# Performance work log

Measured on AMD Instinct MI355X. Metric: run time of the kernel, lower is better.

The kernel has to match this reference:

```python
import jax, jax.numpy as jnp
import numpy as np

B, L, D, H = 2, 2048, 1024, 16
DH = D // H
NEG = -10000.0

def setup_inputs() -> dict:
    key = jax.random.key(0)
    ks = jax.random.split(key, 6)
    scale = 1.0 / np.sqrt(D)
    inp = {
        "x": jax.random.normal(ks[0], (B, L, D), dtype=jnp.float32),
        "m": jnp.ones((B, L), dtype=jnp.int32),  # 1 = valid token, 0 = padded
        "Wq": jax.random.normal(ks[1], (D, D), dtype=jnp.float32) * scale,
        "bq": jnp.zeros((D,), dtype=jnp.float32),
        "Wk": jax.random.normal(ks[2], (D, D), dtype=jnp.float32) * scale,
        "bk": jnp.zeros((D,), dtype=jnp.float32),
        "Wv": jax.random.normal(ks[3], (D, D), dtype=jnp.float32) * scale,
        "bv": jnp.zeros((D,), dtype=jnp.float32),
        "Wp": jax.random.normal(ks[4], (D, D), dtype=jnp.float32) * scale,
        "bp": jnp.zeros((D,), dtype=jnp.float32),
    }
    return inp

def reference(x, m, Wq, bq, Wk, bk, Wv, bv, Wp, bp):
    # torch Linear: x @ W.T + b
    def heads(t):  # (B,L,D) -> (B,H,L,DH)
        return t.reshape(B, L, H, DH).transpose(0, 2, 1, 3)
    q = heads(x @ Wq.T + bq)
    k = heads(x @ Wk.T + bk)
    v = heads(x @ Wv.T + bv)
    att = jnp.einsum("bhqd,bhkd->bhqk", q, k) * (1.0 / np.sqrt(DH))  # (B,H,L,L)
    causal = jnp.tril(jnp.ones((L, L), dtype=bool))[None, None]       # (1,1,L,L)
    att = jnp.where(causal, att, NEG)
    # additive key-padding mask: 0 for valid, -10000 for padded keys
    pad = (1.0 - m.astype(att.dtype))[:, None, None, :] * NEG         # (B,1,1,L)
    att = att + pad
    att = jax.nn.softmax(att, axis=-1)
    y = jnp.einsum("bhqk,bhkd->bhqd", att, v)                          # (B,H,L,DH)
    y = y.transpose(0, 2, 1, 3).reshape(B, L, D)
    return y @ Wp.T + bp
```

## Files before the change

kernel.cpp:

```cpp
#include <hip/hip_runtime.h>
#include <hip/hip_bf16.h>

#define NB 2
#define NL 2048
#define ND 1024
#define NH 16
#define NDH 64
#define NM (NB*NL)

typedef unsigned short u16;
typedef __attribute__((ext_vector_type(8))) short short8;
typedef __attribute__((ext_vector_type(4))) float floatx4;

__device__ __forceinline__ u16 f2bf(float f) {
  union { float f; unsigned int u; } v; v.f = f;
  unsigned int r = v.u + 0x7FFF + ((v.u >> 16) & 1);
  return (u16)(r >> 16);
}

__device__ __forceinline__ void async_cp16(u16* lds, const u16* g) {
  __builtin_amdgcn_global_load_lds(
      (const __attribute__((address_space(1))) void*)g,
      (__attribute__((address_space(3))) void*)lds, 16, 0, 0);
}

__device__ __forceinline__ unsigned dpp_xor1(unsigned v) {
  return (unsigned)__builtin_amdgcn_mov_dpp((int)v, 0xB1, 0xF, 0xF, true);
}

__global__ __launch_bounds__(256)
void cvt_all(const float* __restrict__ wq, const float* __restrict__ wk,
             const float* __restrict__ wv, const float* __restrict__ wp,
             const float* __restrict__ x,
             u16* __restrict__ ow, u16* __restrict__ ox)
{
  const int per4 = ND * ND / 4;
  const int tot  = 4 * per4 + NM * ND / 4;
  for (int t = blockIdx.x * 256 + threadIdx.x; t < tot; t += gridDim.x * 256) {
    const float* src; uint2* dst; int off;
    if (t < 4 * per4) {
      int w = t >> 18; off = t & (per4 - 1);
      src = (w == 0) ? wq : (w == 1) ? wk : (w == 2) ? wv : wp;
      dst = (uint2*)(ow + (size_t)w * ND * ND);
    } else {
      off = t - 4 * per4; src = x; dst = (uint2*)ox;
    }
    float4 f = ((const float4*)src)[off];
    u16 h[4] = { f2bf(f.x), f2bf(f.y), f2bf(f.z), f2bf(f.w) };
    dst[off] = *(const uint2*)h;
  }
}

#define BM 128
#define BN 128
#define BK 32
#define LDT 32

__global__ __launch_bounds__(256)
void gemm_qkv(const u16* __restrict__ A, const u16* __restrict__ Wb,
              const float* __restrict__ bq, const float* __restrict__ bk,
              const float* __restrict__ bv,
              u16* __restrict__ Qb, u16* __restrict__ Kb, u16* __restrict__ Vb)
{
  const int n0g = blockIdx.x * BN;
  const int z   = n0g >> 10;
  const int n0  = n0g & 1023;
  const u16* W    = Wb + (size_t)z * ND * ND;
  const float* Bi = (z == 0) ? bq : (z == 1) ? bk : bv;
  u16* C          = (z == 0) ? Qb : (z == 1) ? Kb : Vb;
  const float sc  = (z == 0) ? 0.125f : 1.0f;

  const int m0 = blockIdx.y * BM;
  const int tid  = threadIdx.x;
  const int lane = tid & 63;
  const int wave = tid >> 6;
  const int wm = (wave >> 1) * 64;
  const int wn = (wave & 1) * 64;
  const int quad = lane >> 4;
  const int l16  = lane & 15;

  __shared__ u16 As[BM * LDT];
  __shared__ u16 Bs[BN * LDT];

  floatx4 acc[4][4];
#pragma unroll
  for (int i = 0; i < 4; ++i)
#pragma unroll
    for (int j = 0; j < 4; ++j)
      acc[i][j] = (floatx4){0.f, 0.f, 0.f, 0.f};

  for (int k0 = 0; k0 < ND; k0 += BK) {
#pragma unroll
    for (int it = 0; it < 2; ++it) {
      int idx = tid + it * 256;
      int rr  = idx >> 2;
      int c8  = (idx & 3) << 3;
      async_cp16(&Bs[idx * 8], &W[(size_t)(n0 + rr) * ND + k0 + c8]);
      async_cp16(&As[idx * 8], &A[(size_t)(m0 + rr) * ND + k0 + c8]);
    }
    __syncthreads();

    short8 af[4], bfr[4];
#pragma unroll
    for (int i = 0; i < 4; ++i)
      af[i] = *(const short8*)&As[(wm + i * 16 + l16) * LDT + quad * 8];
#pragma unroll
    for (int j = 0; j < 4; ++j)
      bfr[j] = *(const short8*)&Bs[(wn + j * 16 + l16) * LDT + quad * 8];

#pragma unroll
    for (int i = 0; i < 4; ++i)
#pragma unroll
      for (int j = 0; j < 4; ++j)
        acc[i][j] = __builtin_amdgcn_mfma_f32_16x16x32_bf16(af[i], bfr[j], acc[i][j], 0, 0, 0);
    __syncthreads();
  }

#pragma unroll
  for (int j = 0; j < 4; ++j) {
    const int ncol = n0 + wn + j * 16 + l16;
    const float bv2 = Bi[ncol];
#pragma unroll
    for (int i = 0; i < 4; ++i) {
      const int mbase = m0 + wm + i * 16 + quad * 4;
#pragma unroll
      for (int r2 = 0; r2 < 4; ++r2) {
        float v = (acc[i][j][r2] + bv2) * sc;
        C[(size_t)(mbase + r2) * ND + ncol] = f2bf(v);
      }
    }
  }
}

#define BN2 64

__global__ __launch_bounds__(256)
void gemm_proj(const u16* __restrict__ A, const u16* __restrict__ W,
               const float* __restrict__ Bi, float* __restrict__ C)
{
  const int n0 = blockIdx.x * BN2;
  const int m0 = blockIdx.y * BM;
  const int tid  = threadIdx.x;
  const int lane = tid & 63;
  const int wave = tid >> 6;
  const int wm = (wave >> 1) * 64;
  const int wn = (wave & 1) * 32;
  const int quad = lane >> 4;
  const int l16  = lane & 15;

  __shared__ u16 As[BM * LDT];
  __shared__ u16 Bs[BN2 * LDT];

  floatx4 acc[4][2];
#pragma unroll
  for (int i = 0; i < 4; ++i)
#pragma unroll
    for (int j = 0; j < 2; ++j)
      acc[i][j] = (floatx4){0.f, 0.f, 0.f, 0.f};

  for (int k0 = 0; k0 < ND; k0 += BK) {
#pragma unroll
    for (int it = 0; it < 2; ++it) {
      int idx = tid + it * 256;
      int rr  = idx >> 2;
      int c8  = (idx & 3) << 3;
      async_cp16(&As[idx * 8], &A[(size_t)(m0 + rr) * ND + k0 + c8]);
    }
    {
      int rr = tid >> 2, c8 = (tid & 3) << 3;
      async_cp16(&Bs[tid * 8], &W[(size_t)(n0 + rr) * ND + k0 + c8]);
    }
    __syncthreads();

    short8 af[4], bfr[2];
#pragma unroll
    for (int i = 0; i < 4; ++i)
      af[i] = *(const short8*)&As[(wm + i * 16 + l16) * LDT + quad * 8];
#pragma unroll
    for (int j = 0; j < 2; ++j)
      bfr[j] = *(const short8*)&Bs[(wn + j * 16 + l16) * LDT + quad * 8];

#pragma unroll
    for (int i = 0; i < 4; ++i)
#pragma unroll
      for (int j = 0; j < 2; ++j)
        acc[i][j] = __builtin_amdgcn_mfma_f32_16x16x32_bf16(af[i], bfr[j], acc[i][j], 0, 0, 0);
    __syncthreads();
  }

#pragma unroll
  for (int j = 0; j < 2; ++j) {
    const int ncol = n0 + wn + j * 16 + l16;
    const float bv2 = Bi[ncol];
#pragma unroll
    for (int i = 0; i < 4; ++i) {
      const int mbase = m0 + wm + i * 16 + quad * 4;
#pragma unroll
      for (int r2 = 0; r2 < 4; ++r2)
        C[(size_t)(mbase + r2) * ND + ncol] = acc[i][j][r2] + bv2;
    }
  }
}

#define KC 64
#define PSTR 72

__global__ __launch_bounds__(256)
void attn_mfma(const u16* __restrict__ Q, const u16* __restrict__ K,
               const u16* __restrict__ V, const int* __restrict__ msk,
               u16* __restrict__ Y)
{
  const int t = blockIdx.x;
  const int r = t >> 8;
  const int xcd = t & 7;
  const int v = (t >> 3) & 31;
  const int bh = xcd * 4 + r;
  const int qt = (r == 0) ? v
               : (r == 1) ? 31 - v
               : (r == 2) ? ((v + 16) & 31)
                          : ((15 - v) & 31);
  const int b = bh >> 4;
  const int h = bh & 15;
  const int q0 = qt * 64;
  const int tid  = threadIdx.x;
  const int lane = tid & 63;
  const int wave = tid >> 6;
  const int wq   = wave * 16;
  const int quad = lane >> 4;
  const int l16  = lane & 15;

  __shared__ u16 Ks[KC][PSTR];
  __shared__ u16 Vt[NDH][PSTR];
  __shared__ u16 Ps[64][PSTR];
  __shared__ u16 Ms[NL];

  const int nchunks = qt + 1;

  for (int j = tid; j < nchunks * KC; j += 256) Ms[j] = (u16)(msk[b * NL + j] ? 1 : 0);

  short8 qf[2];
#pragma unroll
  for (int kk = 0; kk < 2; ++kk)
    qf[kk] = *(const short8*)&Q[(size_t)(b * NL + q0 + wq + l16) * ND
                                + h * NDH + kk * 32 + quad * 8];

  short8 onesf;
  {
    const short ov = (l16 == 0) ? (short)0x3F80 : (short)0;
#pragma unroll
    for (int e = 0; e < 8; ++e) onesf[e] = ov;
  }

  floatx4 o[4];
#pragma unroll
  for (int ot = 0; ot < 4; ++ot) o[ot] = (floatx4){0.f, 0.f, 0.f, 0.f};
  floatx4 lacc = (floatx4){0.f, 0.f, 0.f, 0.f};

  const int odd = l16 & 1;
  for (int kc = 0; kc < nchunks; ++kc) {
    const int k0 = kc * KC;

#pragma unroll
    for (int p = 0; p < 2; ++p) {
      int idx = tid + p * 256;
      int rr = idx >> 3, c = (idx & 7) << 3;
      *(uint4*)&Ks[rr][c] = *(const uint4*)&K[(size_t)(b * NL + k0 + rr) * ND + h * NDH + c];
    }
    {
      int rv = (tid & 31) * 2;
      int c  = (tid >> 5) * 8;
      uint4 va = *(const uint4*)&V[(size_t)(b * NL + k0 + rv)     * ND + h * NDH + c];
      uint4 vb = *(const uint4*)&V[(size_t)(b * NL + k0 + rv + 1) * ND + h * NDH + c];
      const u16* ap = (const u16*)&va;
      const u16* bp = (const u16*)&vb;
#pragma unroll
      for (int e = 0; e < 8; ++e)
        *(unsigned int*)&Vt[c + e][rv] = (unsigned int)ap[e] | ((unsigned int)bp[e] << 16);
    }
    __syncthreads();

    floatx4 sc[4];
#pragma unroll
    for (int ct = 0; ct < 4; ++ct) {
      short8 kf0 = *(const short8*)&Ks[ct * 16 + l16][quad * 8];
      short8 kf1 = *(const short8*)&Ks[ct * 16 + l16][32 + quad * 8];
      floatx4 a = (floatx4){0.f, 0.f, 0.f, 0.f};
      a = __builtin_amdgcn_mfma_f32_16x16x32_bf16(qf[0], kf0, a, 0, 0, 0);
      a = __builtin_amdgcn_mfma_f32_16x16x32_bf16(qf[1], kf1, a, 0, 0, 0);
      sc[ct] = a;
    }

    const bool diag = (kc == qt);
    const int rowb = q0 + wq + quad * 4;
#pragma unroll
    for (int ct = 0; ct < 4; ++ct) {
      const int col = k0 + ct * 16 + l16;
      const float pmul = (float)Ms[col];
      unsigned bb[4];
#pragma unroll
      for (int r2 = 0; r2 < 4; ++r2) {
        float p = pmul * __expf(sc[ct][r2]);
        if (diag) p = (col > rowb + r2) ? 0.f : p;
        bb[r2] = (unsigned)f2bf(p);
      }
      unsigned n0v = dpp_xor1(bb[0]), n1v = dpp_xor1(bb[1]);
      unsigned n2v = dpp_xor1(bb[2]), n3v = dpp_xor1(bb[3]);
      const int colb  = ct * 16 + (l16 & ~1);
      const int row01 = wq + quad * 4 + odd;
      unsigned d01 = odd ? (n1v | (bb[1] << 16)) : (bb[0] | (n0v << 16));
      unsigned d23 = odd ? (n3v | (bb[3] << 16)) : (bb[2] | (n2v << 16));
      *(unsigned*)&Ps[row01][colb]     = d01;
      *(unsigned*)&Ps[row01 + 2][colb] = d23;
    }

#pragma unroll
    for (int kk = 0; kk < 2; ++kk) {
      short8 pf = *(const short8*)&Ps[wq + l16][kk * 32 + quad * 8];
#pragma unroll
      for (int ot = 0; ot < 4; ++ot) {
        short8 vf = *(const short8*)&Vt[ot * 16 + l16][kk * 32 + quad * 8];
        o[ot] = __builtin_amdgcn_mfma_f32_16x16x32_bf16(pf, vf, o[ot], 0, 0, 0);
      }
      lacc = __builtin_amdgcn_mfma_f32_16x16x32_bf16(pf, onesf, lacc, 0, 0, 0);
    }
    __syncthreads();
  }

  float inv[4];
#pragma unroll
  for (int r2 = 0; r2 < 4; ++r2) {
    const float l = __shfl(lacc[r2], quad << 4);
    inv[r2] = 1.0f / l;
  }
#pragma unroll
  for (int ot = 0; ot < 4; ++ot)
#pragma unroll
    for (int r2 = 0; r2 < 4; ++r2) {
      const int row = q0 + wq + quad * 4 + r2;
      Y[(size_t)(b * NL + row) * ND + h * NDH + ot * 16 + l16] = f2bf(o[ot][r2] * inv[r2]);
    }
}

extern "C" void kernel_launch(void* const* d_in, const int* in_sizes, int n_in,
                              void* d_out, int out_size, void* d_ws, size_t ws_size,
                              hipStream_t stream) {
  const float* x  = (const float*)d_in[0];
  const int*   m  = (const int*)d_in[1];
  const float* Wq = (const float*)d_in[2];
  const float* bq = (const float*)d_in[3];
  const float* Wk = (const float*)d_in[4];
  const float* bk = (const float*)d_in[5];
  const float* Wv = (const float*)d_in[6];
  const float* bv = (const float*)d_in[7];
  const float* Wp = (const float*)d_in[8];
  const float* bp = (const float*)d_in[9];
  float* out = (float*)d_out;

  const size_t per = (size_t)NM * ND;
  u16* Qb = (u16*)d_ws;
  u16* Kb = Qb + per;
  u16* Vb = Kb + per;
  u16* Wb = Vb + per;
  u16* Yb = Qb;
  u16* xb = (u16*)d_out;

  cvt_all<<<2048, 256, 0, stream>>>(Wq, Wk, Wv, Wp, x, Wb, xb);

  gemm_qkv<<<dim3(3 * ND / BN, NM / BM), 256, 0, stream>>>(
      xb, Wb, bq, bk, bv, Qb, Kb, Vb);

  attn_mfma<<<1024, 256, 0, stream>>>(Qb, Kb, Vb, m, Yb);

  const u16* Wpb = Wb + 3 * (size_t)ND * ND;
  gemm_proj<<<dim3(ND / BN2, NM / BM), 256, 0, stream>>>(Yb, Wpb, bp, out);
}
```

Baseline: 210.3 us.

## Pre-transpose V and stream K/V into swizzled LDS via async copies

Adds a separate kernel that writes V transposed per head, so the attention kernel can load K and V^T straight into LDS with global_load_lds asynchronous copies instead of register round-trips and scalar transposing stores. The LDS tiles use an XOR swizzle in place of padding to avoid bank conflicts on the fragment reads. The Q scale now folds in log2(e), so exp2 replaces __expf, and the probabilities are packed with the hardware bf16 convert. It costs one extra kernel launch and an extra global round-trip for V, with VT stored in the upper half of the output buffer.

```diff
diff --git a/kernel.cpp b/kernel.cpp
--- a/kernel.cpp
+++ b/kernel.cpp
@@ -12,20 +12,27 @@
 typedef __attribute__((ext_vector_type(8))) short short8;
 typedef __attribute__((ext_vector_type(4))) float floatx4;
 
+#define QSCALE 0.180336880f
+
 __device__ __forceinline__ u16 f2bf(float f) {
   union { float f; unsigned int u; } v; v.f = f;
   unsigned int r = v.u + 0x7FFF + ((v.u >> 16) & 1);
   return (u16)(r >> 16);
 }
 
-__device__ __forceinline__ void async_cp16(u16* lds, const u16* g) {
+__device__ __forceinline__ void async_cp16(const u16* lds, const u16* g) {
   __builtin_amdgcn_global_load_lds(
       (const __attribute__((address_space(1))) void*)g,
       (__attribute__((address_space(3))) void*)lds, 16, 0, 0);
 }
 
-__device__ __forceinline__ unsigned dpp_xor1(unsigned v) {
-  return (unsigned)__builtin_amdgcn_mov_dpp((int)v, 0xB1, 0xF, 0xF, true);
+__device__ __forceinline__ float dpp_xor1_f(float v) {
+  return __int_as_float(__builtin_amdgcn_mov_dpp(__float_as_int(v), 0xB1, 0xF, 0xF, true));
+}
+
+__device__ __forceinline__ unsigned pk_bf16(float lo, float hi) {
+  __hip_bfloat162 h2 = __float22bfloat162_rn(make_float2(lo, hi));
+  return *(unsigned*)&h2;
 }
 
 __global__ __launch_bounds__(256)
@@ -68,7 +75,7 @@
   const u16* W    = Wb + (size_t)z * ND * ND;
   const float* Bi = (z == 0) ? bq : (z == 1) ? bk : bv;
   u16* C          = (z == 0) ? Qb : (z == 1) ? Kb : Vb;
-  const float sc  = (z == 0) ? 0.125f : 1.0f;
+  const float sc  = (z == 0) ? QSCALE : 1.0f;
 
   const int m0 = blockIdx.y * BM;
   const int tid  = threadIdx.x;
@@ -202,12 +209,40 @@
   }
 }
 
+#define TSTR 66
+__global__ __launch_bounds__(256)
+void vtrans(const u16* __restrict__ V, u16* __restrict__ VT)
+{
+  const int lt = blockIdx.x;
+  const int bh = blockIdx.y;
+  const int b = bh >> 4, h = bh & 15;
+  const int l0 = lt * 64;
+  const int tid = threadIdx.x;
+  __shared__ u16 Ls[64][TSTR];
+#pragma unroll
+  for (int p = 0; p < 2; ++p) {
+    int idx = tid + p * 256;
+    int r = idx >> 3, c = (idx & 7) << 3;
+    *(uint4*)&Ls[r][c] = *(const uint4*)&V[(size_t)(b * NL + l0 + r) * ND + h * NDH + c];
+  }
+  __syncthreads();
+#pragma unroll
+  for (int p = 0; p < 2; ++p) {
+    int idx = tid + p * 256;
+    int lg = idx & 7, d = idx >> 3;
+    u16 tb[8];
+#pragma unroll
+    for (int e = 0; e < 8; ++e) tb[e] = Ls[lg * 8 + e][d];
+    *(uint4*)&VT[((size_t)(b * NH + h) * NDH + d) * NL + l0 + lg * 8] = *(const uint4*)tb;
+  }
+}
+
 #define KC 64
 #define PSTR 72
 
 __global__ __launch_bounds__(256)
 void attn_mfma(const u16* __restrict__ Q, const u16* __restrict__ K,
-               const u16* __restrict__ V, const int* __restrict__ msk,
+               const u16* __restrict__ VT, const int* __restrict__ msk,
                u16* __restrict__ Y)
 {
   const int t = blockIdx.x;
@@ -229,14 +264,17 @@
   const int quad = lane >> 4;
   const int l16  = lane & 15;
 
-  __shared__ u16 Ks[KC][PSTR];
-  __shared__ u16 Vt[NDH][PSTR];
+  __shared__ u16 Ks[KC * 64];
+  __shared__ u16 Vt[NDH * 64];
   __shared__ u16 Ps[64][PSTR];
   __shared__ u16 Ms[NL];
 
   const int nchunks = qt + 1;
 
   for (int j = tid; j < nchunks * KC; j += 256) Ms[j] = (u16)(msk[b * NL + j] ? 1 : 0);
+
+  const u16* Kbase  = K  + (size_t)b * NL * ND + h * NDH;
+  const u16* VTbase = VT + (size_t)(b * NH + h) * NDH * NL;
 
   short8 qf[2];
 #pragma unroll
@@ -257,33 +295,27 @@
   floatx4 lacc = (floatx4){0.f, 0.f, 0.f, 0.f};
 
   const int odd = l16 & 1;
+  const int sw  = l16 & 7;
+
   for (int kc = 0; kc < nchunks; ++kc) {
     const int k0 = kc * KC;
 
 #pragma unroll
     for (int p = 0; p < 2; ++p) {
-      int idx = tid + p * 256;
-      int rr = idx >> 3, c = (idx & 7) << 3;
-      *(uint4*)&Ks[rr][c] = *(const uint4*)&K[(size_t)(b * NL + k0 + rr) * ND + h * NDH + c];
-    }
-    {
-      int rv = (tid & 31) * 2;
-      int c  = (tid >> 5) * 8;
-      uint4 va = *(const uint4*)&V[(size_t)(b * NL + k0 + rv)     * ND + h * NDH + c];
-      uint4 vb = *(const uint4*)&V[(size_t)(b * NL + k0 + rv + 1) * ND + h * NDH + c];
-      const u16* ap = (const u16*)&va;
-      const u16* bp = (const u16*)&vb;
-#pragma unroll
-      for (int e = 0; e < 8; ++e)
-        *(unsigned int*)&Vt[c + e][rv] = (unsigned int)ap[e] | ((unsigned int)bp[e] << 16);
+      int sl = tid + p * 256;
+      int rr = sl >> 3;
+      int ch = (sl & 7) ^ (rr & 7);
+      async_cp16(&Ks[sl * 8], Kbase + (size_t)(k0 + rr) * ND + ch * 8);
+      async_cp16(&Vt[sl * 8], VTbase + (size_t)rr * NL + k0 + ch * 8);
     }
     __syncthreads();
 
     floatx4 sc[4];
 #pragma unroll
     for (int ct = 0; ct < 4; ++ct) {
-      short8 kf0 = *(const short8*)&Ks[ct * 16 + l16][quad * 8];
-      short8 kf1 = *(const short8*)&Ks[ct * 16 + l16][32 + quad * 8];
+      const u16* krow = &Ks[(ct * 16 + l16) * 64];
+      short8 kf0 = *(const short8*)(krow + ((quad ^ sw) << 3));
+      short8 kf1 = *(const short8*)(krow + (((4 | quad) ^ sw) << 3));
       floatx4 a = (floatx4){0.f, 0.f, 0.f, 0.f};
       a = __builtin_amdgcn_mfma_f32_16x16x32_bf16(qf[0], kf0, a, 0, 0, 0);
       a = __builtin_amdgcn_mfma_f32_16x16x32_bf16(qf[1], kf1, a, 0, 0, 0);
@@ -296,19 +328,19 @@
     for (int ct = 0; ct < 4; ++ct) {
       const int col = k0 + ct * 16 + l16;
       const float pmul = (float)Ms[col];
-      unsigned bb[4];
+      float pv[4];
 #pragma unroll
       for (int r2 = 0; r2 < 4; ++r2) {
-        float p = pmul * __expf(sc[ct][r2]);
+        float p = pmul * __builtin_amdgcn_exp2f(sc[ct][r2]);
         if (diag) p = (col > rowb + r2) ? 0.f : p;
-        bb[r2] = (unsigned)f2bf(p);
+        pv[r2] = p;
       }
-      unsigned n0v = dpp_xor1(bb[0]), n1v = dpp_xor1(bb[1]);
-      unsigned n2v = dpp_xor1(bb[2]), n3v = dpp_xor1(bb[3]);
+      float nb0 = dpp_xor1_f(pv[0]), nb1 = dpp_xor1_f(pv[1]);
+      float nb2 = dpp_xor1_f(pv[2]), nb3 = dpp_xor1_f(pv[3]);
       const int colb  = ct * 16 + (l16 & ~1);
       const int row01 = wq + quad * 4 + odd;
-      unsigned d01 = odd ? (n1v | (bb[1] << 16)) : (bb[0] | (n0v << 16));
-      unsigned d23 = odd ? (n3v | (bb[3] << 16)) : (bb[2] | (n2v << 16));
+      unsigned d01 = odd ? pk_bf16(nb1, pv[1]) : pk_bf16(pv[0], nb0);
+      unsigned d23 = odd ? pk_bf16(nb3, pv[3]) : pk_bf16(pv[2], nb2);
       *(unsigned*)&Ps[row01][colb]     = d01;
       *(unsigned*)&Ps[row01 + 2][colb] = d23;
     }
@@ -318,7 +350,8 @@
       short8 pf = *(const short8*)&Ps[wq + l16][kk * 32 + quad * 8];
 #pragma unroll
       for (int ot = 0; ot < 4; ++ot) {
-        short8 vf = *(const short8*)&Vt[ot * 16 + l16][kk * 32 + quad * 8];
+        const u16* vrow = &Vt[(ot * 16 + l16) * 64];
+        short8 vf = *(const short8*)(vrow + ((((kk << 2) | quad) ^ sw) << 3));
         o[ot] = __builtin_amdgcn_mfma_f32_16x16x32_bf16(pf, vf, o[ot], 0, 0, 0);
       }
       lacc = __builtin_amdgcn_mfma_f32_16x16x32_bf16(pf, onesf, lacc, 0, 0, 0);
@@ -363,13 +396,16 @@
   u16* Wb = Vb + per;
   u16* Yb = Qb;
   u16* xb = (u16*)d_out;
+  u16* VTb = xb + per;
 
   cvt_all<<<2048, 256, 0, stream>>>(Wq, Wk, Wv, Wp, x, Wb, xb);
 
   gemm_qkv<<<dim3(3 * ND / BN, NM / BM), 256, 0, stream>>>(
       xb, Wb, bq, bk, bv, Qb, Kb, Vb);
 
-  attn_mfma<<<1024, 256, 0, stream>>>(Qb, Kb, Vb, m, Yb);
+  vtrans<<<dim3(NL / 64, NB * NH), 256, 0, stream>>>(Vb, VTb);
+
+  attn_mfma<<<1024, 256, 0, stream>>>(Qb, Kb, VTb, m, Yb);
 
   const u16* Wpb = Wb + 3 * (size_t)ND * ND;
   gemm_proj<<<dim3(ND / BN2, NM / BM), 256, 0, stream>>>(Yb, Wpb, bp, out);
```

Measured after the change: 195.5 us. -7.0%, faster.
